# Optimization experiments

Hardware: AMD Instinct MI355X
Metric: run time of the kernel (lower is better)

The kernel has to match this reference:

```python
import jax, jax.numpy as jnp
import numpy as np

N = 8192

def setup_inputs() -> dict:
    key = jax.random.key(0)
    k1, k2, k3 = jax.random.split(key, 3)
    logRR = jax.random.normal(k1, (N, 1), dtype=jnp.float32)
    ytime = jax.random.uniform(k2, (N,), dtype=jnp.float32, minval=0.01, maxval=10.0)
    ystatus = (jax.random.uniform(k3, (N,), dtype=jnp.float32) < 0.7).astype(jnp.float32)
    return {"logRR": logRR, "ytime": ytime, "ystatus": ystatus}

def reference(logRR, ytime, ystatus):
    # Cox partial-likelihood loss (cox-nnet formulation).
    theta = logRR.reshape(-1)                      # [N]
    exp_theta = jnp.exp(theta)                     # [N]
    # Risk-set mask: R[i, j] = 1 if ytime[j] >= ytime[i]
    R = (ytime[None, :] >= ytime[:, None]).astype(theta.dtype)  # [N, N]
    risk_sum = R @ exp_theta                       # [N], sum_j exp(theta_j) over risk set of i
    loss = -jnp.mean((theta - jnp.log(risk_sum)) * ystatus)
    return loss
```

## Files before the change

### kernel.cpp

```cpp
#include <hip/hip_runtime.h>
#include <math.h>

#define N        8192
#define NBLK     512
#define THREADS  256
#define IPB      16
#define SLICES   16
#define G4       (N / 4)

__global__ __launch_bounds__(THREADS, 2) void cox_fused(
        const float* __restrict__ logRR,
        const float* __restrict__ ytime,
        const float* __restrict__ ystatus,
        float* __restrict__ ws) {
    __shared__ float s_yt[N];
    __shared__ float s_et[N];
    __shared__ float s_red[THREADS];

    const int tid = threadIdx.x;
    const int b   = blockIdx.x;

    const float4* ytg = reinterpret_cast<const float4*>(ytime);
    const float4* thg = reinterpret_cast<const float4*>(logRR);
    float4* syt = reinterpret_cast<float4*>(s_yt);
    float4* set = reinterpret_cast<float4*>(s_et);
#pragma unroll
    for (int k = 0; k < G4 / THREADS; ++k) {
        int idx = k * THREADS + tid;
        float4 y = ytg[idx];
        float4 t = thg[idx];
        syt[idx] = y;
        float4 e;
        e.x = __expf(t.x); e.y = __expf(t.y);
        e.z = __expf(t.z); e.w = __expf(t.w);
        set[idx] = e;
    }
    __syncthreads();

    const int il = tid & (IPB - 1);
    const int sl = tid >> 4;
    const float yti = ytime[b * IPB + il];

    float s0 = 0.f, s1 = 0.f, s2 = 0.f, s3 = 0.f;
#pragma unroll 8
    for (int m = 0; m < G4 / SLICES; ++m) {
        int jg = m * SLICES + sl;
        float4 yt = syt[jg];
        float4 et = set[jg];
        s0 += (yt.x >= yti) ? et.x : 0.f;
        s1 += (yt.y >= yti) ? et.y : 0.f;
        s2 += (yt.z >= yti) ? et.z : 0.f;
        s3 += (yt.w >= yti) ? et.w : 0.f;
    }
    s_red[tid] = (s0 + s1) + (s2 + s3);
    __syncthreads();

    if (tid < IPB) {
        float risk = 0.f;
#pragma unroll
        for (int k = 0; k < SLICES; ++k) risk += s_red[k * IPB + tid];
        const int i = b * IPB + tid;
        float lv = (logRR[i] - logf(risk)) * ystatus[i];
#pragma unroll
        for (int off = 8; off; off >>= 1) lv += __shfl_down(lv, off, 16);
        if (tid == 0) ws[b] = lv;
    }
}

__global__ __launch_bounds__(512) void cox_final(
        const float* __restrict__ ws, float* __restrict__ out) {
    const int tid = threadIdx.x;
    float v = ws[tid];
#pragma unroll
    for (int off = 32; off; off >>= 1) v += __shfl_down(v, off);
    __shared__ float red[8];
    if ((tid & 63) == 0) red[tid >> 6] = v;
    __syncthreads();
    if (tid == 0) {
        float s = 0.f;
#pragma unroll
        for (int w = 0; w < 8; ++w) s += red[w];
        out[0] = -s / (float)N;
    }
}

extern "C" void kernel_launch(void* const* d_in, const int* in_sizes, int n_in,
                              void* d_out, int out_size, void* d_ws, size_t ws_size,
                              hipStream_t stream) {
    const float* logRR   = (const float*)d_in[0];
    const float* ytime   = (const float*)d_in[1];
    const float* ystatus = (const float*)d_in[2];
    float* out = (float*)d_out;
    float* ws  = (float*)d_ws;

    cox_fused<<<NBLK, THREADS, 0, stream>>>(logRR, ytime, ystatus, ws);
    cox_final<<<1, 512, 0, stream>>>(ws, out);
}
```

Baseline: 16.20 us.

## Register-block 8 rows per thread to reuse LDS loads across comparisons

Each thread now handles 8 row thresholds instead of 1, so every float4 pair loaded from LDS feeds 32 compare-adds rather than 4. This cuts LDS traffic per useful operation. Partial sums are reduced with wave-level xor shuffles before a smaller shared-memory reduction. logf is also swapped for the faster __logf. The cost is more registers per thread, which may lower occupancy.

After: 15.14 us. -6.5%, faster.

```diff
diff --git a/kernel.cpp b/kernel.cpp
--- a/kernel.cpp
+++ b/kernel.cpp
@@ -5,8 +5,11 @@
 #define NBLK     512
 #define THREADS  256
 #define IPB      16
-#define SLICES   16
+#define R        8
+#define ITH      (IPB / R)
+#define SLICES   (THREADS / ITH)
 #define G4       (N / 4)
+#define MITER    (G4 / SLICES)
 
 __global__ __launch_bounds__(THREADS, 2) void cox_fused(
         const float* __restrict__ logRR,
@@ -15,7 +18,7 @@
         float* __restrict__ ws) {
     __shared__ float s_yt[N];
     __shared__ float s_et[N];
-    __shared__ float s_red[THREADS];
+    __shared__ float s_red[(THREADS / 64) * ITH * R];
 
     const int tid = threadIdx.x;
     const int b   = blockIdx.x;
@@ -37,30 +40,59 @@
     }
     __syncthreads();
 
-    const int il = tid & (IPB - 1);
-    const int sl = tid >> 4;
-    const float yti = ytime[b * IPB + il];
+    const int it = tid & (ITH - 1);
+    const int sl = tid >> 1;
 
-    float s0 = 0.f, s1 = 0.f, s2 = 0.f, s3 = 0.f;
-#pragma unroll 8
-    for (int m = 0; m < G4 / SLICES; ++m) {
+    float yti[R];
+#pragma unroll
+    for (int r = 0; r < R; ++r) yti[r] = ytime[b * IPB + it * R + r];
+
+    float acc[R][2] = {};
+#pragma unroll 4
+    for (int m = 0; m < MITER; ++m) {
         int jg = m * SLICES + sl;
         float4 yt = syt[jg];
         float4 et = set[jg];
-        s0 += (yt.x >= yti) ? et.x : 0.f;
-        s1 += (yt.y >= yti) ? et.y : 0.f;
-        s2 += (yt.z >= yti) ? et.z : 0.f;
-        s3 += (yt.w >= yti) ? et.w : 0.f;
+#pragma unroll
+        for (int r = 0; r < R; ++r) {
+            float a0 = acc[r][0], a1 = acc[r][1];
+            a0 += (yt.x >= yti[r]) ? et.x : 0.f;
+            a1 += (yt.y >= yti[r]) ? et.y : 0.f;
+            a0 += (yt.z >= yti[r]) ? et.z : 0.f;
+            a1 += (yt.w >= yti[r]) ? et.w : 0.f;
+            acc[r][0] = a0; acc[r][1] = a1;
+        }
     }
-    s_red[tid] = (s0 + s1) + (s2 + s3);
+
+    const int wave = tid >> 6;
+    const int lane = tid & 63;
+    float red[R];
+#pragma unroll
+    for (int r = 0; r < R; ++r) {
+        float v = acc[r][0] + acc[r][1];
+        v += __shfl_xor(v, 2);
+        v += __shfl_xor(v, 4);
+        v += __shfl_xor(v, 8);
+        v += __shfl_xor(v, 16);
+        v += __shfl_xor(v, 32);
+        red[r] = v;
+    }
+    if (lane < ITH) {
+#pragma unroll
+        for (int r = 0; r < R; ++r)
+            s_red[(wave * ITH + lane) * R + r] = red[r];
+    }
     __syncthreads();
 
     if (tid < IPB) {
+        const int itl = tid >> 3;
+        const int rl  = tid & 7;
         float risk = 0.f;
 #pragma unroll
-        for (int k = 0; k < SLICES; ++k) risk += s_red[k * IPB + tid];
+        for (int w = 0; w < THREADS / 64; ++w)
+            risk += s_red[(w * ITH + itl) * R + rl];
         const int i = b * IPB + tid;
-        float lv = (logRR[i] - logf(risk)) * ystatus[i];
+        float lv = (logRR[i] - __logf(risk)) * ystatus[i];
 #pragma unroll
         for (int off = 8; off; off >>= 1) lv += __shfl_down(lv, off, 16);
         if (tid == 0) ws[b] = lv;
```
